# Optimization experiments

Hardware: AMD Instinct MI355X
Metric: run time of the kernel (lower is better)

The kernel has to match this reference:

```python
import jax, jax.numpy as jnp
import numpy as np

N_NODES = 100000
N_EDGES = 1600000
IN_SIZE = 128
HIDDEN = 32
OUT_SIZE = 16


def _mean_agg(h, src, dst, n_nodes):
    # segment-sum of source features into destination nodes, then divide by in-degree
    summed = jax.ops.segment_sum(h[src], dst, num_segments=n_nodes)  # [N, D]
    deg = jax.ops.segment_sum(jnp.ones((src.shape[0],), h.dtype), dst, num_segments=n_nodes)
    return summed / jnp.maximum(deg, 1.0)[:, None]


def _sage_layer(h, src, dst, W_self, W_neigh, b):
    # DGL SAGEConv (mean): fc_self(h) + fc_neigh(mean_neigh(h)) + bias
    agg = _mean_agg(h, src, dst, h.shape[0])
    return h @ W_self + agg @ W_neigh + b


def setup_inputs() -> dict:
    key = jax.random.key(0)
    ks = jax.random.split(key, 9)
    inp = {
        "x": jax.random.normal(ks[0], (N_NODES, IN_SIZE), jnp.float32),
        "edge_src": jax.random.randint(ks[1], (N_EDGES,), 0, N_NODES, jnp.int32),
        "edge_dst": jax.random.randint(ks[2], (N_EDGES,), 0, N_NODES, jnp.int32),
        "W_self1": jax.random.normal(ks[3], (IN_SIZE, HIDDEN), jnp.float32) / np.sqrt(IN_SIZE),
        "W_neigh1": jax.random.normal(ks[4], (IN_SIZE, HIDDEN), jnp.float32) / np.sqrt(IN_SIZE),
        "b1": jnp.zeros((HIDDEN,), jnp.float32),
        "W_self2": jax.random.normal(ks[5], (HIDDEN, HIDDEN), jnp.float32) / np.sqrt(HIDDEN),
        "W_neigh2": jax.random.normal(ks[6], (HIDDEN, HIDDEN), jnp.float32) / np.sqrt(HIDDEN),
        "b2": jnp.zeros((HIDDEN,), jnp.float32),
        "W_self3": jax.random.normal(ks[7], (HIDDEN, OUT_SIZE), jnp.float32) / np.sqrt(HIDDEN),
        "W_neigh3": jax.random.normal(ks[8], (HIDDEN, OUT_SIZE), jnp.float32) / np.sqrt(HIDDEN),
        "b3": jnp.zeros((OUT_SIZE,), jnp.float32),
    }
    return inp


def reference(x, edge_src, edge_dst,
              W_self1, W_neigh1, b1,
              W_self2, W_neigh2, b2,
              W_self3, W_neigh3, b3):
    h = jax.nn.relu(_sage_layer(x, edge_src, edge_dst, W_self1, W_neigh1, b1))
    h = jax.nn.relu(_sage_layer(h, edge_src, edge_dst, W_self2, W_neigh2, b2))
    h = _sage_layer(h, edge_src, edge_dst, W_self3, W_neigh3, b3)
    return h
```

## Files before the change

### kernel.cpp

```cpp
#include <hip/hip_runtime.h>


#define BLOCK 256
#define NBLK 256
#define BSH 9
#define CAP 12288

__global__ void hist_kernel(const int* __restrict__ dst, int* __restrict__ hist,
                            int n_edges, int nbuk, int ch) {
    __shared__ int cnt[256];
    int tid = threadIdx.x;
    for (int i = tid; i < nbuk; i += BLOCK) cnt[i] = 0;
    __syncthreads();
    int e0 = blockIdx.x * ch;
    int e1 = e0 + ch; if (e1 > n_edges) e1 = n_edges;
    for (int e = e0 + tid; e < e1; e += BLOCK)
        atomicAdd(&cnt[dst[e] >> BSH], 1);
    __syncthreads();
    for (int i = tid; i < nbuk; i += BLOCK)
        hist[i * NBLK + blockIdx.x] = cnt[i];
}

__global__ void scanBlk_kernel(int* __restrict__ hist, int* __restrict__ buktot) {
    int b = blockIdx.x;
    int tid = threadIdx.x;
    int orig = hist[b * NBLK + tid];
    int v = orig;
    int lane = tid & 63, w = tid >> 6;
#pragma unroll
    for (int off = 1; off < 64; off <<= 1) {
        int u = __shfl_up(v, off);
        if (lane >= off) v += u;
    }
    __shared__ int wps[4];
    if (lane == 63) wps[w] = v;
    __syncthreads();
    int wadd = 0;
    for (int k = 0; k < w; ++k) wadd += wps[k];
    int excl = v - orig + wadd;
    hist[b * NBLK + tid] = excl;
    if (tid == 255) buktot[b] = excl + orig;
}

__global__ void scanBuk_kernel(const int* __restrict__ buktot, int* __restrict__ bukoff,
                               int nbuk, int* __restrict__ startp, int n_nodes, int n_edges) {
    int tid = threadIdx.x;
    int orig = (tid < nbuk) ? buktot[tid] : 0;
    int v = orig;
    int lane = tid & 63, w = tid >> 6;
#pragma unroll
    for (int off = 1; off < 64; off <<= 1) {
        int u = __shfl_up(v, off);
        if (lane >= off) v += u;
    }
    __shared__ int wps[4];
    if (lane == 63) wps[w] = v;
    __syncthreads();
    int wadd = 0;
    for (int k = 0; k < w; ++k) wadd += wps[k];
    int excl = v - orig + wadd;
    if (tid < nbuk) bukoff[tid] = excl;
    if (tid == 0) { bukoff[nbuk] = n_edges; startp[n_nodes] = n_edges; }
}

__global__ void part_kernel(const int* __restrict__ src, const int* __restrict__ dst,
                            const int* __restrict__ hist, const int* __restrict__ bukoff,
                            int2* __restrict__ pairs, int n_edges, int nbuk, int ch) {
    __shared__ int base[256];
    __shared__ int cnt[256];
    int tid = threadIdx.x;
    for (int i = tid; i < nbuk; i += BLOCK) {
        base[i] = hist[i * NBLK + blockIdx.x] + bukoff[i];
        cnt[i] = 0;
    }
    __syncthreads();
    int e0 = blockIdx.x * ch;
    int e1 = e0 + ch; if (e1 > n_edges) e1 = n_edges;
    for (int e = e0 + tid; e < e1; e += BLOCK) {
        int d = dst[e];
        int b = d >> BSH;
        int r = atomicAdd(&cnt[b], 1);
        pairs[base[b] + r] = make_int2(src[e], d);
    }
}

__global__ void build_kernel(const int2* __restrict__ pairs, const int* __restrict__ bukoff,
                             int* __restrict__ start, float* __restrict__ invdeg,
                             int* __restrict__ csr_src, int n_nodes) {
    __shared__ int deg[512];
    __shared__ int lst[512];
    __shared__ int cur[512];
    __shared__ int wps[4];
    __shared__ int scsr[CAP];

    int b = blockIdx.x;
    int tid = threadIdx.x;
    int e0 = bukoff[b];
    int e1 = bukoff[b + 1];
    int lo = b << BSH;
    int hi = lo + (1 << BSH); if (hi > n_nodes) hi = n_nodes;
    int nn = hi - lo;
    int ne = e1 - e0;

    for (int i = tid; i < 512; i += BLOCK) deg[i] = 0;
    __syncthreads();
    for (int i = e0 + tid; i < e1; i += BLOCK)
        atomicAdd(&deg[pairs[i].y - lo], 1);
    __syncthreads();

    int d0 = deg[2 * tid], d1 = deg[2 * tid + 1];
    int s = d0 + d1;
    int lane = tid & 63, w = tid >> 6;
    int v = s;
#pragma unroll
    for (int off = 1; off < 64; off <<= 1) {
        int u = __shfl_up(v, off);
        if (lane >= off) v += u;
    }
    if (lane == 63) wps[w] = v;
    __syncthreads();
    int wb = 0;
    for (int k = 0; k < w; ++k) wb += wps[k];
    int excl = wb + v - s;
    lst[2 * tid] = excl;
    lst[2 * tid + 1] = excl + d0;
    cur[2 * tid] = 0;
    cur[2 * tid + 1] = 0;
    __syncthreads();

    for (int i = tid; i < nn; i += BLOCK) {
        start[lo + i] = e0 + lst[i];
        int d = deg[i];
        invdeg[lo + i] = 1.0f / (float)(d < 1 ? 1 : d);
    }

    if (ne <= CAP) {
        for (int i = e0 + tid; i < e1; i += BLOCK) {
            int2 pr = pairs[i];
            int dl = pr.y - lo;
            int sl = lst[dl] + atomicAdd(&cur[dl], 1);
            scsr[sl] = pr.x;
        }
        __syncthreads();
        for (int i = tid; i < ne; i += BLOCK) csr_src[e0 + i] = scsr[i];
    } else {
        for (int i = e0 + tid; i < e1; i += BLOCK) {
            int2 pr = pairs[i];
            int dl = pr.y - lo;
            int sl = lst[dl] + atomicAdd(&cur[dl], 1);
            csr_src[e0 + sl] = pr.x;
        }
    }
}

template<int DIN, int DOUT, int OPT, int NPT>
__global__ __launch_bounds__(256, 4)
void proj_reg(const float* __restrict__ h,
              const float* __restrict__ Ws,
              const float* __restrict__ Wn,
              const float* __restrict__ bias,
              float* __restrict__ pre,
              float* __restrict__ p,
              int n_nodes) {
    constexpr int OD  = 2 * DOUT;
    constexpr int OG  = OD / OPT;
    constexpr int NG  = 256 / OG;
    constexpr int NT  = NPT * NG;
    constexpr int NV  = OPT / 4;

    __shared__ float sW[DIN][OD];
    __shared__ float sb[DOUT];

    const int tid = threadIdx.x;
    for (int i = tid; i < DIN * OD; i += 256) {
        int k = i / OD, o = i % OD;
        sW[k][o] = (o < DOUT) ? Ws[k * DOUT + o] : Wn[k * DOUT + (o - DOUT)];
    }
    if (tid < DOUT) sb[tid] = bias[tid];
    __syncthreads();

    const int to = tid % OG;
    const int tn = tid / OG;
    const int o0 = to * OPT;
    const int node0 = blockIdx.x * NT + tn * NPT;

    const float4* __restrict__ xp[NPT];
#pragma unroll
    for (int n = 0; n < NPT; ++n) {
        int node = node0 + n;
        int safe = (node < n_nodes) ? node : (n_nodes - 1);
        xp[n] = reinterpret_cast<const float4*>(h + (size_t)safe * DIN);
    }

    float acc[NPT][OPT];
#pragma unroll
    for (int n = 0; n < NPT; ++n)
#pragma unroll
        for (int o = 0; o < OPT; ++o) acc[n][o] = 0.f;

#pragma unroll 2
    for (int k4 = 0; k4 < DIN / 4; ++k4) {
        float4 xv[NPT];
#pragma unroll
        for (int n = 0; n < NPT; ++n) xv[n] = xp[n][k4];
#pragma unroll
        for (int kk = 0; kk < 4; ++kk) {
            int k = 4 * k4 + kk;
            float4 w[NV];
#pragma unroll
            for (int v = 0; v < NV; ++v)
                w[v] = *reinterpret_cast<const float4*>(&sW[k][o0 + 4 * v]);
#pragma unroll
            for (int n = 0; n < NPT; ++n) {
                float xk = reinterpret_cast<const float*>(&xv[n])[kk];
#pragma unroll
                for (int v = 0; v < NV; ++v) {
                    acc[n][4 * v + 0] = fmaf(xk, w[v].x, acc[n][4 * v + 0]);
                    acc[n][4 * v + 1] = fmaf(xk, w[v].y, acc[n][4 * v + 1]);
                    acc[n][4 * v + 2] = fmaf(xk, w[v].z, acc[n][4 * v + 2]);
                    acc[n][4 * v + 3] = fmaf(xk, w[v].w, acc[n][4 * v + 3]);
                }
            }
        }
    }

    const bool self_half = (o0 < DOUT);
    const int oo = self_half ? o0 : (o0 - DOUT);
    float* __restrict__ dstbuf = self_half ? pre : p;
#pragma unroll
    for (int n = 0; n < NPT; ++n) {
        int node = node0 + n;
        if (node >= n_nodes) continue;
#pragma unroll
        for (int v = 0; v < NV; ++v) {
            float4 r;
            r.x = acc[n][4 * v + 0];
            r.y = acc[n][4 * v + 1];
            r.z = acc[n][4 * v + 2];
            r.w = acc[n][4 * v + 3];
            if (self_half) {
                r.x += sb[oo + 4 * v + 0];
                r.y += sb[oo + 4 * v + 1];
                r.z += sb[oo + 4 * v + 2];
                r.w += sb[oo + 4 * v + 3];
            }
            *reinterpret_cast<float4*>(dstbuf + (size_t)node * DOUT + oo + 4 * v) = r;
        }
    }
}

template<int D, bool RELU>
__global__ void gather_kernel(const float* __restrict__ p,
                              const int* __restrict__ csr_src,
                              const int* __restrict__ start,
                              const float* __restrict__ pre,
                              const float* __restrict__ invdeg,
                              float* __restrict__ out,
                              int n_nodes) {
    constexpr int LPN = D / 4;
    constexpr int NPG = 64 / LPN;
    int wave = threadIdx.x >> 6;
    int lane = threadIdx.x & 63;
    int g = blockIdx.x * (blockDim.x >> 6) + wave;
    if (g >= n_nodes) return;
    int sub = lane / LPN;
    int fl  = lane % LPN;
    int s0 = start[g];
    int s1 = start[g + 1];
    const float4* __restrict__ p4 = reinterpret_cast<const float4*>(p);
    float4 a0 = make_float4(0.f, 0.f, 0.f, 0.f);
    float4 a1 = make_float4(0.f, 0.f, 0.f, 0.f);
    int j = s0 + sub;
    for (; j + NPG < s1; j += 2 * NPG) {
        int c0 = csr_src[j];
        int c1 = csr_src[j + NPG];
        float4 v0 = p4[c0 * LPN + fl];
        float4 v1 = p4[c1 * LPN + fl];
        a0.x += v0.x; a0.y += v0.y; a0.z += v0.z; a0.w += v0.w;
        a1.x += v1.x; a1.y += v1.y; a1.z += v1.z; a1.w += v1.w;
    }
    if (j < s1) {
        float4 v = p4[csr_src[j] * LPN + fl];
        a0.x += v.x; a0.y += v.y; a0.z += v.z; a0.w += v.w;
    }
    float4 a = make_float4(a0.x + a1.x, a0.y + a1.y, a0.z + a1.z, a0.w + a1.w);
#pragma unroll
    for (int off = 32; off >= LPN; off >>= 1) {
        a.x += __shfl_down(a.x, off);
        a.y += __shfl_down(a.y, off);
        a.z += __shfl_down(a.z, off);
        a.w += __shfl_down(a.w, off);
    }
    if (lane < LPN) {
        float id = invdeg[g];
        float4 pr = reinterpret_cast<const float4*>(pre)[g * LPN + fl];
        float4 r;
        r.x = pr.x + a.x * id;
        r.y = pr.y + a.y * id;
        r.z = pr.z + a.z * id;
        r.w = pr.w + a.w * id;
        if (RELU) {
            r.x = fmaxf(r.x, 0.f); r.y = fmaxf(r.y, 0.f);
            r.z = fmaxf(r.z, 0.f); r.w = fmaxf(r.w, 0.f);
        }
        reinterpret_cast<float4*>(out)[g * LPN + fl] = r;
    }
}

extern "C" void kernel_launch(void* const* d_in, const int* in_sizes, int n_in,
                              void* d_out, int out_size, void* d_ws, size_t ws_size,
                              hipStream_t stream) {
    const float* x        = (const float*)d_in[0];
    const int*   edge_src = (const int*)d_in[1];
    const int*   edge_dst = (const int*)d_in[2];
    const float* Ws1 = (const float*)d_in[3];
    const float* Wn1 = (const float*)d_in[4];
    const float* b1  = (const float*)d_in[5];
    const float* Ws2 = (const float*)d_in[6];
    const float* Wn2 = (const float*)d_in[7];
    const float* b2  = (const float*)d_in[8];
    const float* Ws3 = (const float*)d_in[9];
    const float* Wn3 = (const float*)d_in[10];
    const float* b3  = (const float*)d_in[11];
    float* out = (float*)d_out;

    const int IN = 128, HID = 32;
    const int n_nodes = in_sizes[0] / IN;
    const int n_edges = in_sizes[1];
    const int nbuk = (n_nodes + (1 << BSH) - 1) >> BSH;
    const int ch   = (n_edges + NBLK - 1) / NBLK;

    char* wsb = (char*)d_ws;
    size_t off = 0;
    auto alloc = [&](size_t bytes) { char* r = wsb + off; off = (off + bytes + 255) & ~(size_t)255; return r; };
    int*   startp = (int*)alloc(((size_t)n_nodes + 1) * sizeof(int));
    float* invdeg = (float*)alloc((size_t)n_nodes * sizeof(float));
    int*   csr    = (int*)alloc((size_t)n_edges * sizeof(int));
    int*   hist   = (int*)alloc((size_t)nbuk * NBLK * sizeof(int));
    int*   buktot = (int*)alloc(256 * sizeof(int));
    int*   bukoff = (int*)alloc(257 * sizeof(int));
    float* B0     = (float*)alloc((size_t)n_nodes * HID * sizeof(float));
    float* B1     = (float*)alloc((size_t)n_nodes * HID * sizeof(float));
    float* B3     = (float*)alloc((size_t)n_nodes * HID * sizeof(float));
    int2*  pairs  = (int2*)B0;

    const int gP    = (n_nodes + 63) / 64;
    const int gGat  = (n_nodes + 3) / 4;

    hist_kernel   <<<NBLK, BLOCK, 0, stream>>>(edge_dst, hist, n_edges, nbuk, ch);
    scanBlk_kernel<<<nbuk, BLOCK, 0, stream>>>(hist, buktot);
    scanBuk_kernel<<<1, BLOCK, 0, stream>>>(buktot, bukoff, nbuk, startp, n_nodes, n_edges);
    part_kernel   <<<NBLK, BLOCK, 0, stream>>>(edge_src, edge_dst, hist, bukoff, pairs, n_edges, nbuk, ch);
    build_kernel  <<<nbuk, BLOCK, 0, stream>>>(pairs, bukoff, startp, invdeg, csr, n_nodes);

    proj_reg<128, 32, 8, 2><<<gP, BLOCK, 0, stream>>>(x, Ws1, Wn1, b1, B0, B1, n_nodes);
    gather_kernel<32, true><<<gGat, BLOCK, 0, stream>>>(B1, csr, startp, B0, invdeg, B3, n_nodes);

    proj_reg<32, 32, 8, 2><<<gP, BLOCK, 0, stream>>>(B3, Ws2, Wn2, b2, B0, B1, n_nodes);
    gather_kernel<32, true><<<gGat, BLOCK, 0, stream>>>(B1, csr, startp, B0, invdeg, B3, n_nodes);

    proj_reg<32, 16, 4, 2><<<gP, BLOCK, 0, stream>>>(B3, Ws3, Wn3, b3, B0, B1, n_nodes);
    gather_kernel<16, false><<<gGat, BLOCK, 0, stream>>>(B1, csr, startp, B0, invdeg, out, n_nodes);
}
```

Baseline: 216.9 us.

## Pack edge pairs into 32-bit words and retile projection to 4x4 register blocks

The partition step now stores each edge as one 32-bit word: a 20-bit source index plus the 9-bit local destination offset within its bucket. This halves the traffic of the intermediate pairs buffer written by part_kernel and read twice by build_kernel, but it assumes node ids fit in 20 bits. The projection kernel is retiled so each thread computes 4 nodes by 4 outputs, with the next weight row prefetched from shared memory into registers, which changes the grid size for the last layer. Gather indexing is widened to size_t.

```diff
diff --git a/kernel.cpp b/kernel.cpp
--- a/kernel.cpp
+++ b/kernel.cpp
@@ -65,7 +65,7 @@
 
 __global__ void part_kernel(const int* __restrict__ src, const int* __restrict__ dst,
                             const int* __restrict__ hist, const int* __restrict__ bukoff,
-                            int2* __restrict__ pairs, int n_edges, int nbuk, int ch) {
+                            unsigned* __restrict__ pairs, int n_edges, int nbuk, int ch) {
     __shared__ int base[256];
     __shared__ int cnt[256];
     int tid = threadIdx.x;
@@ -79,12 +79,13 @@
     for (int e = e0 + tid; e < e1; e += BLOCK) {
         int d = dst[e];
         int b = d >> BSH;
+        unsigned dl = (unsigned)(d & ((1 << BSH) - 1));
         int r = atomicAdd(&cnt[b], 1);
-        pairs[base[b] + r] = make_int2(src[e], d);
-    }
-}
-
-__global__ void build_kernel(const int2* __restrict__ pairs, const int* __restrict__ bukoff,
+        pairs[base[b] + r] = (unsigned)src[e] | (dl << 20);
+    }
+}
+
+__global__ void build_kernel(const unsigned* __restrict__ pairs, const int* __restrict__ bukoff,
                              int* __restrict__ start, float* __restrict__ invdeg,
                              int* __restrict__ csr_src, int n_nodes) {
     __shared__ int deg[512];
@@ -105,7 +106,7 @@
     for (int i = tid; i < 512; i += BLOCK) deg[i] = 0;
     __syncthreads();
     for (int i = e0 + tid; i < e1; i += BLOCK)
-        atomicAdd(&deg[pairs[i].y - lo], 1);
+        atomicAdd(&deg[pairs[i] >> 20], 1);
     __syncthreads();
 
     int d0 = deg[2 * tid], d1 = deg[2 * tid + 1];
@@ -136,24 +137,24 @@
 
     if (ne <= CAP) {
         for (int i = e0 + tid; i < e1; i += BLOCK) {
-            int2 pr = pairs[i];
-            int dl = pr.y - lo;
+            unsigned pr = pairs[i];
+            int dl = pr >> 20;
             int sl = lst[dl] + atomicAdd(&cur[dl], 1);
-            scsr[sl] = pr.x;
+            scsr[sl] = (int)(pr & 0xFFFFFu);
         }
         __syncthreads();
         for (int i = tid; i < ne; i += BLOCK) csr_src[e0 + i] = scsr[i];
     } else {
         for (int i = e0 + tid; i < e1; i += BLOCK) {
-            int2 pr = pairs[i];
-            int dl = pr.y - lo;
+            unsigned pr = pairs[i];
+            int dl = pr >> 20;
             int sl = lst[dl] + atomicAdd(&cur[dl], 1);
-            csr_src[e0 + sl] = pr.x;
-        }
-    }
-}
-
-template<int DIN, int DOUT, int OPT, int NPT>
+            csr_src[e0 + sl] = (int)(pr & 0xFFFFFu);
+        }
+    }
+}
+
+template<int DIN, int DOUT>
 __global__ __launch_bounds__(256, 4)
 void proj_reg(const float* __restrict__ h,
               const float* __restrict__ Ws,
@@ -163,10 +164,9 @@
               float* __restrict__ p,
               int n_nodes) {
     constexpr int OD  = 2 * DOUT;
-    constexpr int OG  = OD / OPT;
+    constexpr int OG  = OD / 4;
     constexpr int NG  = 256 / OG;
-    constexpr int NT  = NPT * NG;
-    constexpr int NV  = OPT / 4;
+    constexpr int NT  = 4 * NG;
 
     __shared__ float sW[DIN][OD];
     __shared__ float sb[DOUT];
@@ -181,46 +181,43 @@
 
     const int to = tid % OG;
     const int tn = tid / OG;
-    const int o0 = to * OPT;
-    const int node0 = blockIdx.x * NT + tn * NPT;
-
-    const float4* __restrict__ xp[NPT];
-#pragma unroll
-    for (int n = 0; n < NPT; ++n) {
+    const int o0 = to * 4;
+    const int node0 = blockIdx.x * NT + tn * 4;
+
+    const float4* __restrict__ xp[4];
+#pragma unroll
+    for (int n = 0; n < 4; ++n) {
         int node = node0 + n;
         int safe = (node < n_nodes) ? node : (n_nodes - 1);
         xp[n] = reinterpret_cast<const float4*>(h + (size_t)safe * DIN);
     }
 
-    float acc[NPT][OPT];
-#pragma unroll
-    for (int n = 0; n < NPT; ++n)
-#pragma unroll
-        for (int o = 0; o < OPT; ++o) acc[n][o] = 0.f;
-
+    float acc[4][4];
+#pragma unroll
+    for (int n = 0; n < 4; ++n)
+#pragma unroll
+        for (int o = 0; o < 4; ++o) acc[n][o] = 0.f;
+
+    float4 wcur = *reinterpret_cast<const float4*>(&sW[0][o0]);
 #pragma unroll 2
     for (int k4 = 0; k4 < DIN / 4; ++k4) {
-        float4 xv[NPT];
-#pragma unroll
-        for (int n = 0; n < NPT; ++n) xv[n] = xp[n][k4];
+        float4 xv[4];
+#pragma unroll
+        for (int n = 0; n < 4; ++n) xv[n] = xp[n][k4];
 #pragma unroll
         for (int kk = 0; kk < 4; ++kk) {
             int k = 4 * k4 + kk;
-            float4 w[NV];
-#pragma unroll
-            for (int v = 0; v < NV; ++v)
-                w[v] = *reinterpret_cast<const float4*>(&sW[k][o0 + 4 * v]);
-#pragma unroll
-            for (int n = 0; n < NPT; ++n) {
+            float4 wnext = (k + 1 < DIN)
+                ? *reinterpret_cast<const float4*>(&sW[k + 1][o0]) : wcur;
+#pragma unroll
+            for (int n = 0; n < 4; ++n) {
                 float xk = reinterpret_cast<const float*>(&xv[n])[kk];
-#pragma unroll
-                for (int v = 0; v < NV; ++v) {
-                    acc[n][4 * v + 0] = fmaf(xk, w[v].x, acc[n][4 * v + 0]);
-                    acc[n][4 * v + 1] = fmaf(xk, w[v].y, acc[n][4 * v + 1]);
-                    acc[n][4 * v + 2] = fmaf(xk, w[v].z, acc[n][4 * v + 2]);
-                    acc[n][4 * v + 3] = fmaf(xk, w[v].w, acc[n][4 * v + 3]);
-                }
+                acc[n][0] = fmaf(xk, wcur.x, acc[n][0]);
+                acc[n][1] = fmaf(xk, wcur.y, acc[n][1]);
+                acc[n][2] = fmaf(xk, wcur.z, acc[n][2]);
+                acc[n][3] = fmaf(xk, wcur.w, acc[n][3]);
             }
+            wcur = wnext;
         }
     }
 
@@ -228,24 +225,16 @@
     const int oo = self_half ? o0 : (o0 - DOUT);
     float* __restrict__ dstbuf = self_half ? pre : p;
 #pragma unroll
-    for (int n = 0; n < NPT; ++n) {
+    for (int n = 0; n < 4; ++n) {
         int node = node0 + n;
         if (node >= n_nodes) continue;
-#pragma unroll
-        for (int v = 0; v < NV; ++v) {
-            float4 r;
-            r.x = acc[n][4 * v + 0];
-            r.y = acc[n][4 * v + 1];
-            r.z = acc[n][4 * v + 2];
-            r.w = acc[n][4 * v + 3];
-            if (self_half) {
-                r.x += sb[oo + 4 * v + 0];
-                r.y += sb[oo + 4 * v + 1];
-                r.z += sb[oo + 4 * v + 2];
-                r.w += sb[oo + 4 * v + 3];
-            }
-            *reinterpret_cast<float4*>(dstbuf + (size_t)node * DOUT + oo + 4 * v) = r;
-        }
+        float4 r;
+        r.x = acc[n][0]; r.y = acc[n][1]; r.z = acc[n][2]; r.w = acc[n][3];
+        if (self_half) {
+            r.x += sb[oo + 0]; r.y += sb[oo + 1];
+            r.z += sb[oo + 2]; r.w += sb[oo + 3];
+        }
+        *reinterpret_cast<float4*>(dstbuf + (size_t)node * DOUT + oo) = r;
     }
 }
 
@@ -274,13 +263,13 @@
     for (; j + NPG < s1; j += 2 * NPG) {
         int c0 = csr_src[j];
         int c1 = csr_src[j + NPG];
-        float4 v0 = p4[c0 * LPN + fl];
-        float4 v1 = p4[c1 * LPN + fl];
+        float4 v0 = p4[(size_t)c0 * LPN + fl];
+        float4 v1 = p4[(size_t)c1 * LPN + fl];
         a0.x += v0.x; a0.y += v0.y; a0.z += v0.z; a0.w += v0.w;
         a1.x += v1.x; a1.y += v1.y; a1.z += v1.z; a1.w += v1.w;
     }
     if (j < s1) {
-        float4 v = p4[csr_src[j] * LPN + fl];
+        float4 v = p4[(size_t)csr_src[j] * LPN + fl];
         a0.x += v.x; a0.y += v.y; a0.z += v.z; a0.w += v.w;
     }
     float4 a = make_float4(a0.x + a1.x, a0.y + a1.y, a0.z + a1.z, a0.w + a1.w);
@@ -293,7 +282,7 @@
     }
     if (lane < LPN) {
         float id = invdeg[g];
-        float4 pr = reinterpret_cast<const float4*>(pre)[g * LPN + fl];
+        float4 pr = reinterpret_cast<const float4*>(pre)[(size_t)g * LPN + fl];
         float4 r;
         r.x = pr.x + a.x * id;
         r.y = pr.y + a.y * id;
@@ -303,7 +292,7 @@
             r.x = fmaxf(r.x, 0.f); r.y = fmaxf(r.y, 0.f);
             r.z = fmaxf(r.z, 0.f); r.w = fmaxf(r.w, 0.f);
         }
-        reinterpret_cast<float4*>(out)[g * LPN + fl] = r;
+        reinterpret_cast<float4*>(out)[(size_t)g * LPN + fl] = r;
     }
 }
 
@@ -342,9 +331,10 @@
     float* B0     = (float*)alloc((size_t)n_nodes * HID * sizeof(float));
     float* B1     = (float*)alloc((size_t)n_nodes * HID * sizeof(float));
     float* B3     = (float*)alloc((size_t)n_nodes * HID * sizeof(float));
-    int2*  pairs  = (int2*)B0;
-
-    const int gP    = (n_nodes + 63) / 64;
+    unsigned* pairs = (unsigned*)B0;
+
+    const int gP12  = (n_nodes + 63) / 64;
+    const int gP3   = (n_nodes + 127) / 128;
     const int gGat  = (n_nodes + 3) / 4;
 
     hist_kernel   <<<NBLK, BLOCK, 0, stream>>>(edge_dst, hist, n_edges, nbuk, ch);
@@ -353,12 +343,12 @@
     part_kernel   <<<NBLK, BLOCK, 0, stream>>>(edge_src, edge_dst, hist, bukoff, pairs, n_edges, nbuk, ch);
     build_kernel  <<<nbuk, BLOCK, 0, stream>>>(pairs, bukoff, startp, invdeg, csr, n_nodes);
 
-    proj_reg<128, 32, 8, 2><<<gP, BLOCK, 0, stream>>>(x, Ws1, Wn1, b1, B0, B1, n_nodes);
+    proj_reg<128, 32><<<gP12, BLOCK, 0, stream>>>(x, Ws1, Wn1, b1, B0, B1, n_nodes);
     gather_kernel<32, true><<<gGat, BLOCK, 0, stream>>>(B1, csr, startp, B0, invdeg, B3, n_nodes);
 
-    proj_reg<32, 32, 8, 2><<<gP, BLOCK, 0, stream>>>(B3, Ws2, Wn2, b2, B0, B1, n_nodes);
+    proj_reg<32, 32><<<gP12, BLOCK, 0, stream>>>(B3, Ws2, Wn2, b2, B0, B1, n_nodes);
     gather_kernel<32, true><<<gGat, BLOCK, 0, stream>>>(B1, csr, startp, B0, invdeg, B3, n_nodes);
 
-    proj_reg<32, 16, 4, 2><<<gP, BLOCK, 0, stream>>>(B3, Ws3, Wn3, b3, B0, B1, n_nodes);
+    proj_reg<32, 16><<<gP3, BLOCK, 0, stream>>>(B3, Ws3, Wn3, b3, B0, B1, n_nodes);
     gather_kernel<16, false><<<gGat, BLOCK, 0, stream>>>(B1, csr, startp, B0, invdeg, out, n_nodes);
 }
```

New measurement: 262.6 us. 1.21x slower.
